# Performance work log

Hardware: AMD Instinct MI355X
Metric: run time of the kernel (lower is better)

The kernel has to match this reference:

```python
import jax, jax.numpy as jnp
import numpy as np

SUPPORT = 1
NEIGHBOR = 20
STRIDE = 2
BS, V = 4, 2048


def _gather(feat, idx):
    # feat: (b, v, c), idx: (b, v, n) -> (b, v, n, c)
    b = feat.shape[0]
    return feat[jnp.arange(b)[:, None, None], idx]


def get_neighbor_index(vertices, k):
    # pairwise squared distances, take k nearest excluding self
    inner = jnp.einsum('bid,bjd->bij', vertices, vertices)
    sq = jnp.sum(vertices * vertices, axis=-1)
    dist = sq[:, :, None] - 2.0 * inner + sq[:, None, :]
    _, idx = jax.lax.top_k(-dist, k + 1)
    return idx[:, :, 1:]


def conv_layer(w, b, d, nbr, vertices, fmap, out_c):
    bs, v, n = nbr.shape
    diff = _gather(vertices, nbr) - vertices[:, :, None, :]  # (b,v,n,3)
    diff = diff / jnp.maximum(jnp.linalg.norm(diff, axis=-1, keepdims=True), 1e-12)
    dirn = d / jnp.maximum(jnp.linalg.norm(d, axis=0, keepdims=True), 1e-12)
    theta = jnp.einsum('bvnd,de->bvne', diff, dirn)  # (b,v,n,S*out)
    feat = fmap @ w + b  # (b,v,(S+1)*out)
    center = feat[..., :out_c]
    support = _gather(feat[..., out_c:], nbr)  # (b,v,n,S*out)
    act = (theta * support).reshape(bs, v, n, SUPPORT, out_c)
    act = jnp.sum(jnp.max(act, axis=2), axis=2)  # max over neighbors, sum over supports
    return center + act


LAYERS = [('c0', 3, 32), ('c1', 32, 64), ('c12', 64, 64), ('c13', 64, 64), ('c14', 64, 64),
          ('p1', 64, 64), ('c2', 64, 128), ('c3', 128, 256), ('c4', 256, 1024),
          ('c42', 1024, 1024), ('c43', 1024, 1024), ('c44', 1024, 1024)]


def _layer_params(key, in_c, out_c):
    k1, k2, k3 = jax.random.split(key, 3)
    stdv = 1.0 / np.sqrt((SUPPORT + 1) * out_c)
    w = jax.random.uniform(k1, (in_c, (SUPPORT + 1) * out_c), minval=-stdv, maxval=stdv, dtype=jnp.float32)
    b = jax.random.uniform(k2, ((SUPPORT + 1) * out_c,), minval=-stdv, maxval=stdv, dtype=jnp.float32)
    d = jax.random.uniform(k3, (3, SUPPORT * out_c), minval=-stdv, maxval=stdv, dtype=jnp.float32)
    return w, b, d


def setup_inputs() -> dict:
    key = jax.random.key(0)
    keys = jax.random.split(key, 20)
    inp = {'vertices': jax.random.normal(keys[0], (BS, V, 3), dtype=jnp.float32)}
    for i, (name, ic, oc) in enumerate(LAYERS):
        w, b, d = _layer_params(keys[i + 1], ic, oc)
        inp[name + '_w'], inp[name + '_b'], inp[name + '_d'] = w, b, d
    inp['fc1_w'] = jax.random.normal(keys[14], (1024, 256), dtype=jnp.float32) * 0.02
    inp['fc1_b'] = jnp.zeros((256,), jnp.float32)
    inp['bn_g'] = jnp.ones((256,), jnp.float32)
    inp['bn_b'] = jnp.zeros((256,), jnp.float32)
    inp['fc2_w'] = jax.random.normal(keys[15], (256, 40), dtype=jnp.float32) * 0.02
    inp['fc2_b'] = jnp.zeros((40,), jnp.float32)
    return inp


def reference(vertices, c0_w, c0_b, c0_d, c1_w, c1_b, c1_d, c12_w, c12_b, c12_d, c13_w, c13_b, c13_d, c14_w, c14_b, c14_d, p1_w, p1_b, p1_d, c2_w, c2_b, c2_d, c3_w, c3_b, c3_d, c4_w, c4_b, c4_d, c42_w, c42_b, c42_d, c43_w, c43_b, c43_d, c44_w, c44_b, c44_d, fc1_w, fc1_b, bn_g, bn_b, fc2_w, fc2_b):
    nbr = get_neighbor_index(vertices, NEIGHBOR)
    fm = conv_layer(c0_w, c0_b, c0_d, nbr, vertices, vertices, 32)
    fm = conv_layer(c1_w, c1_b, c1_d, nbr, vertices, fm, 64)
    fm = conv_layer(c12_w, c12_b, c12_d, nbr, vertices, fm, 64)
    fm = conv_layer(c13_w, c13_b, c13_d, nbr, vertices, fm, 64)
    fm = conv_layer(c14_w, c14_b, c14_d, nbr, vertices, fm, 64)
    # pool_1: conv, neighbor-max pooling, stride-2 vertex subsampling
    fm = conv_layer(p1_w, p1_b, p1_d, nbr, vertices, fm, 64)
    fm = jnp.max(_gather(fm, nbr), axis=2)
    sub = jnp.arange(0, vertices.shape[1], STRIDE)
    vertices2 = vertices[:, sub]
    fm = fm[:, sub]
    nbr2 = get_neighbor_index(vertices2, NEIGHBOR)
    fm = conv_layer(c2_w, c2_b, c2_d, nbr2, vertices2, fm, 128)
    fm = conv_layer(c3_w, c3_b, c3_d, nbr2, vertices2, fm, 256)
    fm = conv_layer(c4_w, c4_b, c4_d, nbr2, vertices2, fm, 1024)
    fm = conv_layer(c42_w, c42_b, c42_d, nbr2, vertices2, fm, 1024)
    fm = conv_layer(c43_w, c43_b, c43_d, nbr2, vertices2, fm, 1024)
    fm = conv_layer(c44_w, c44_b, c44_d, nbr2, vertices2, fm, 1024)
    g = jnp.max(fm, axis=1)  # (b, 1024) global max pool
    h = g @ fc1_w + fc1_b  # dropout = identity in eval
    h = h * jax.lax.rsqrt(jnp.float32(1.0 + 1e-5)) * bn_g + bn_b  # BN eval, running mean 0 / var 1
    h = jax.nn.relu(h)
    return h @ fc2_w + fc2_b
```

## Files before the change

### kernel.cpp

```cpp
#include <hip/hip_runtime.h>
#include <float.h>
#include <math.h>

#define BS 4
#define V1 2048
#define V2 1024
#define NB 20
#define KSEL 21

typedef __attribute__((ext_vector_type(8))) short short8v;
typedef __attribute__((ext_vector_type(4))) float f32x4;

__device__ __forceinline__ unsigned short f2bf(float x) {
    union { float f; unsigned u; } v; v.f = x;
    unsigned r = (v.u + 0x7fffu + ((v.u >> 16) & 1u)) >> 16;
    return (unsigned short)r;
}
__device__ __forceinline__ float bf2f(unsigned short h) {
    return __uint_as_float((unsigned)h << 16);
}
__device__ __forceinline__ unsigned umin32(unsigned a, unsigned b) { return a < b ? a : b; }

__device__ __forceinline__ void gload16(const void* g, void* l) {
    __builtin_amdgcn_global_load_lds((const __attribute__((address_space(1))) void*)g,
                                     (__attribute__((address_space(3))) void*)l, 16, 0, 0);
}

template<int SLOTS>
__global__ __launch_bounds__(256)
void knn_wave_kernel(const float* __restrict__ verts, int stride, int* __restrict__ nbr)
{
    constexpr int Vv = SLOTS * 64;
    __shared__ float xs[Vv], ys[Vv], zs[Vv];
    int tid = threadIdx.x;
    int lane = tid & 63;
    int wv = tid >> 6;
    int b = blockIdx.x / (Vv / 4);
    int q0 = (blockIdx.x % (Vv / 4)) * 4;
    const float* vb = verts + (size_t)b * V1 * 3;
    for (int p = tid; p < Vv; p += 256) {
        xs[p] = vb[(size_t)p * stride * 3 + 0];
        ys[p] = vb[(size_t)p * stride * 3 + 1];
        zs[p] = vb[(size_t)p * stride * 3 + 2];
    }
    __syncthreads();
    int i = q0 + wv;
    float xi = xs[i], yi = ys[i], zi = zs[i];
    float sqi = xi * xi + yi * yi + zi * zi;
    unsigned keys[SLOTS];
    #pragma unroll
    for (int s = 0; s < SLOTS; ++s) {
        int j = s * 64 + lane;
        float xj = xs[j], yj = ys[j], zj = zs[j];
        float sqj = xj * xj + yj * yj + zj * zj;
        float d = sqi - 2.0f * (xi * xj + yi * yj + zi * zj) + sqj;
        unsigned u = __float_as_uint(d);
        u = (u & 0x80000000u) ? ~u : (u | 0x80000000u);
        keys[s] = (u & ~31u) | (unsigned)s;
    }
    const unsigned UMAX = 0xFFFFFFFFu;
    unsigned c0 = UMAX, c1 = UMAX, c2 = UMAX, c3 = UMAX;
    #pragma unroll
    for (int s = 0; s < SLOTS; ++s) c0 = umin32(c0, keys[s]);
    #pragma unroll
    for (int s = 0; s < SLOTS; ++s) { unsigned k = keys[s]; if (k > c0) c1 = umin32(c1, k); }
    #pragma unroll
    for (int s = 0; s < SLOTS; ++s) { unsigned k = keys[s]; if (k > c1) c2 = umin32(c2, k); }
    #pragma unroll
    for (int s = 0; s < SLOTS; ++s) { unsigned k = keys[s]; if (k > c2) c3 = umin32(c3, k); }

    unsigned lm = c0;
    int* out = nbr + ((size_t)b * Vv + i) * NB;
    for (int it = 0; it < KSEL; ++it) {
        unsigned m = lm;
        #pragma unroll
        for (int off = 1; off < 64; off <<= 1)
            m = umin32(m, (unsigned)__shfl_xor((int)m, off));
        unsigned long long bal = __ballot(lm == m);
        int wl = __ffsll(bal) - 1;
        int slot = (int)(m & 31u);
        int j = slot * 64 + wl;
        if (it > 0 && lane == 0) out[it - 1] = j;
        if (lane == wl) {
            c0 = c1; c1 = c2; c2 = c3; c3 = UMAX;
            if (c0 == UMAX) {
                #pragma unroll
                for (int s = 0; s < SLOTS; ++s) {
                    unsigned k = keys[s];
                    if (k > m) c0 = umin32(c0, k);
                }
            }
            lm = c0;
        }
    }
}

__global__ __launch_bounds__(256)
void diffn_kernel(const float* __restrict__ verts, const int* __restrict__ nbr,
                  int Vv, int stride, float* __restrict__ diffn)
{
    int t = blockIdx.x * 256 + threadIdx.x;
    int total = BS * Vv * NB;
    if (t >= total) return;
    int v = (t / NB) % Vv;
    int b = t / (NB * Vv);
    const float* vb = verts + (size_t)b * V1 * 3;
    int j = nbr[t];
    float xi = vb[(size_t)v * stride * 3 + 0];
    float yi = vb[(size_t)v * stride * 3 + 1];
    float zi = vb[(size_t)v * stride * 3 + 2];
    float dx = vb[(size_t)j * stride * 3 + 0] - xi;
    float dy = vb[(size_t)j * stride * 3 + 1] - yi;
    float dz = vb[(size_t)j * stride * 3 + 2] - zi;
    float nrm = sqrtf(dx * dx + dy * dy + dz * dz);
    float inv = 1.0f / fmaxf(nrm, 1e-12f);
    diffn[(size_t)t * 3 + 0] = dx * inv;
    diffn[(size_t)t * 3 + 1] = dy * inv;
    diffn[(size_t)t * 3 + 2] = dz * inv;
}

__global__ __launch_bounds__(256)
void convT_kernel(const float* __restrict__ W, unsigned short* __restrict__ Wt, int K, int N)
{
    __shared__ float t[32][33];
    int k0 = blockIdx.y * 32, n0 = blockIdx.x * 32;
    int tx = threadIdx.x % 32, ty = threadIdx.x / 32;
    #pragma unroll
    for (int r = ty; r < 32; r += 8) t[r][tx] = W[(size_t)(k0 + r) * N + n0 + tx];
    __syncthreads();
    #pragma unroll
    for (int r = ty; r < 32; r += 8) Wt[(size_t)(n0 + r) * K + k0 + tx] = f2bf(t[tx][r]);
}

__global__ __launch_bounds__(256)
void c0_kernel(const float* __restrict__ verts, const float* __restrict__ W,
               const float* __restrict__ Bv, unsigned short* __restrict__ feat)
{
    int t = blockIdx.x * 256 + threadIdx.x;
    if (t >= BS * V1 * 64) return;
    int n = t & 63, m = t >> 6;
    float x = verts[(size_t)m * 3 + 0];
    float y = verts[(size_t)m * 3 + 1];
    float z = verts[(size_t)m * 3 + 2];
    feat[t] = f2bf(x * W[n] + y * W[64 + n] + z * W[128 + n] + Bv[n]);
}

template<int BK>
__global__ __launch_bounds__(256)
void gemm_mfma(const unsigned short* __restrict__ A, const unsigned short* __restrict__ Wt,
               const float* __restrict__ bias, unsigned short* __restrict__ C,
               int M, int N, int K)
{
    constexpr int RB = BK * 2;
    constexpr int TILE_B = 128 * RB;
    constexpr int SWM = (BK == 64) ? 7 : 3;
    __shared__ __align__(16) char smem[2 * TILE_B];
    int tid = threadIdx.x;
    int lane = tid & 63, wid = tid >> 6;
    int wr = wid >> 1, wc = wid & 1;
    int m0 = blockIdx.y * 128, n0 = blockIdx.x * 128;

    f32x4 acc[4][4] = {};

    constexpr int rounds = TILE_B / 4096;
    int srow[rounds], soffe[rounds];
    #pragma unroll
    for (int r = 0; r < rounds; ++r) {
        int L = r * 4096 + tid * 16;
        int row = L / RB;
        int off = (L % RB) ^ ((row & SWM) << 4);
        srow[r] = row; soffe[r] = off >> 1;
    }

    for (int kt = 0; kt < K; kt += BK) {
        #pragma unroll
        for (int r = 0; r < rounds; ++r)
            gload16(A + (size_t)(m0 + srow[r]) * K + kt + soffe[r],
                    smem + r * 4096 + wid * 1024);
        #pragma unroll
        for (int r = 0; r < rounds; ++r)
            gload16(Wt + (size_t)(n0 + srow[r]) * K + kt + soffe[r],
                    smem + TILE_B + r * 4096 + wid * 1024);
        asm volatile("s_waitcnt vmcnt(0)" ::: "memory");
        __syncthreads();
        #pragma unroll
        for (int ks = 0; ks < BK / 32; ++ks) {
            short8v av[4], bv[4];
            #pragma unroll
            for (int i = 0; i < 4; ++i) {
                int row = wr * 64 + i * 16 + (lane & 15);
                int off = (ks * 64 + ((lane >> 4) * 16)) ^ ((row & SWM) << 4);
                av[i] = *(const short8v*)(smem + row * RB + off);
            }
            #pragma unroll
            for (int j = 0; j < 4; ++j) {
                int row = wc * 64 + j * 16 + (lane & 15);
                int off = (ks * 64 + ((lane >> 4) * 16)) ^ ((row & SWM) << 4);
                bv[j] = *(const short8v*)(smem + TILE_B + row * RB + off);
            }
            #pragma unroll
            for (int i = 0; i < 4; ++i)
                #pragma unroll
                for (int j = 0; j < 4; ++j)
                    acc[i][j] = __builtin_amdgcn_mfma_f32_16x16x32_bf16(av[i], bv[j], acc[i][j], 0, 0, 0);
        }
        __syncthreads();
    }
    #pragma unroll
    for (int i = 0; i < 4; ++i) {
        #pragma unroll
        for (int j = 0; j < 4; ++j) {
            int col = n0 + wc * 64 + j * 16 + (lane & 15);
            int rowb = m0 + wr * 64 + i * 16 + ((lane >> 4) * 4);
            float bv2 = bias[col];
            #pragma unroll
            for (int v = 0; v < 4; ++v)
                C[(size_t)(rowb + v) * N + col] = f2bf(acc[i][j][v] + bv2);
        }
    }
}

__global__ __launch_bounds__(256)
void act_kernel(const unsigned short* __restrict__ feat, const int* __restrict__ nbr,
                const float* __restrict__ diffn, const float* __restrict__ dmat,
                float* __restrict__ outp, unsigned short* __restrict__ outh,
                int Vv, int OC)
{
    int OC4 = OC >> 2;
    int t = blockIdx.x * 256 + threadIdx.x;
    int total = BS * Vv * OC4;
    if (t >= total) return;
    int c4 = t % OC4;
    int v = (t / OC4) % Vv;
    int b = t / (OC4 * Vv);
    const float4* d4 = (const float4*)dmat;
    float4 D0 = d4[c4], D1 = d4[OC4 + c4], D2 = d4[2 * OC4 + c4];
    float n0 = sqrtf(D0.x * D0.x + D1.x * D1.x + D2.x * D2.x);
    float n1 = sqrtf(D0.y * D0.y + D1.y * D1.y + D2.y * D2.y);
    float n2 = sqrtf(D0.z * D0.z + D1.z * D1.z + D2.z * D2.z);
    float n3 = sqrtf(D0.w * D0.w + D1.w * D1.w + D2.w * D2.w);
    float i0 = 1.0f / fmaxf(n0, 1e-12f);
    float i1 = 1.0f / fmaxf(n1, 1e-12f);
    float i2 = 1.0f / fmaxf(n2, 1e-12f);
    float i3 = 1.0f / fmaxf(n3, 1e-12f);
    D0.x *= i0; D0.y *= i1; D0.z *= i2; D0.w *= i3;
    D1.x *= i0; D1.y *= i1; D1.z *= i2; D1.w *= i3;
    D2.x *= i0; D2.y *= i1; D2.z *= i2; D2.w *= i3;

    const int* nb = nbr + ((size_t)b * Vv + v) * NB;
    const float* dfn = diffn + ((size_t)b * Vv + v) * NB * 3;
    const ushort4* frow = (const ushort4*)feat;
    size_t rowstride = (size_t)(2 * OC4);
    const ushort4* fsup = frow + (size_t)b * Vv * rowstride + OC4 + c4;
    float4 m = make_float4(-FLT_MAX, -FLT_MAX, -FLT_MAX, -FLT_MAX);
    for (int n = 0; n < NB; ++n) {
        int idx = nb[n];
        float e0 = dfn[3 * n + 0], e1 = dfn[3 * n + 1], e2 = dfn[3 * n + 2];
        ushort4 s = fsup[(size_t)idx * rowstride];
        float th;
        th = e0 * D0.x + e1 * D1.x + e2 * D2.x; m.x = fmaxf(m.x, th * bf2f(s.x));
        th = e0 * D0.y + e1 * D1.y + e2 * D2.y; m.y = fmaxf(m.y, th * bf2f(s.y));
        th = e0 * D0.z + e1 * D1.z + e2 * D2.z; m.z = fmaxf(m.z, th * bf2f(s.z));
        th = e0 * D0.w + e1 * D1.w + e2 * D2.w; m.w = fmaxf(m.w, th * bf2f(s.w));
    }
    ushort4 cen = frow[(size_t)b * Vv * rowstride + (size_t)v * rowstride + c4];
    float4 r = make_float4(bf2f(cen.x) + m.x, bf2f(cen.y) + m.y,
                           bf2f(cen.z) + m.z, bf2f(cen.w) + m.w);
    size_t oidx = ((size_t)b * Vv + v) * OC4 + c4;
    ushort4 h;
    h.x = f2bf(r.x); h.y = f2bf(r.y); h.z = f2bf(r.z); h.w = f2bf(r.w);
    ((ushort4*)outh)[oidx] = h;
    if (outp) ((float4*)outp)[oidx] = r;
}

__global__ __launch_bounds__(256)
void pool_kernel(const ushort4* __restrict__ fmh, const int* __restrict__ nbr,
                 ushort4* __restrict__ outp)
{
    const int C4 = 16;
    int t = blockIdx.x * 256 + threadIdx.x;
    int total = BS * V2 * C4;
    if (t >= total) return;
    int c = t % C4;
    int v2 = (t / C4) % V2;
    int b = t / (C4 * V2);
    const int* nb = nbr + ((size_t)b * V1 + 2 * v2) * NB;
    float4 m = make_float4(-FLT_MAX, -FLT_MAX, -FLT_MAX, -FLT_MAX);
    for (int n = 0; n < NB; ++n) {
        int idx = nb[n];
        ushort4 s = fmh[((size_t)b * V1 + idx) * C4 + c];
        m.x = fmaxf(m.x, bf2f(s.x)); m.y = fmaxf(m.y, bf2f(s.y));
        m.z = fmaxf(m.z, bf2f(s.z)); m.w = fmaxf(m.w, bf2f(s.w));
    }
    ushort4 h;
    h.x = f2bf(m.x); h.y = f2bf(m.y); h.z = f2bf(m.z); h.w = f2bf(m.w);
    outp[((size_t)b * V2 + v2) * C4 + c] = h;
}

__global__ __launch_bounds__(256)
void gmax_part(const float* __restrict__ fm, float* __restrict__ part)
{
    int c = blockIdx.x * 256 + threadIdx.x;
    int ch = blockIdx.y;
    int b = blockIdx.z;
    float m = -FLT_MAX;
    for (int v = ch * 128; v < (ch + 1) * 128; ++v)
        m = fmaxf(m, fm[((size_t)b * V2 + v) * 1024 + c]);
    part[((size_t)b * 8 + ch) * 1024 + c] = m;
}

__global__ __launch_bounds__(256)
void gmax_final(const float* __restrict__ part, float* __restrict__ g)
{
    int t = blockIdx.x * 256 + threadIdx.x;
    if (t >= BS * 1024) return;
    int c = t % 1024, b = t / 1024;
    float m = -FLT_MAX;
    for (int ch = 0; ch < 8; ++ch)
        m = fmaxf(m, part[((size_t)b * 8 + ch) * 1024 + c]);
    g[t] = m;
}

__global__ __launch_bounds__(256)
void fc1_part(const float* __restrict__ g, const float* __restrict__ fc1w,
              float* __restrict__ hpart)
{
    int b = blockIdx.x, kg = blockIdx.y;
    int j = threadIdx.x;
    __shared__ float gs[128];
    if (j < 128) gs[j] = g[(size_t)b * 1024 + kg * 128 + j];
    __syncthreads();
    float h = 0.0f;
    #pragma unroll 4
    for (int k = 0; k < 128; ++k)
        h = fmaf(gs[k], fc1w[(size_t)(kg * 128 + k) * 256 + j], h);
    hpart[((size_t)b * 8 + kg) * 256 + j] = h;
}

__global__ __launch_bounds__(256)
void head2_kernel(const float* __restrict__ hpart, const float* __restrict__ fc1b,
                  const float* __restrict__ bng, const float* __restrict__ bnb,
                  const float* __restrict__ fc2w, const float* __restrict__ fc2b,
                  float* __restrict__ outp)
{
    __shared__ float hs[256];
    __shared__ float part[4][40];
    int b = blockIdx.x;
    int j = threadIdx.x;
    float s = fc1b[j];
    #pragma unroll
    for (int kg = 0; kg < 8; ++kg) s += hpart[((size_t)b * 8 + kg) * 256 + j];
    const float rc = 0.99999500003749937f;
    s = s * rc * bng[j] + bnb[j];
    hs[j] = fmaxf(s, 0.0f);
    __syncthreads();
    int ks = j >> 6, jo = j & 63;
    if (jo < 40) {
        float o = 0.0f;
        for (int k = ks * 64; k < ks * 64 + 64; ++k)
            o = fmaf(hs[k], fc2w[(size_t)k * 40 + jo], o);
        part[ks][jo] = o;
    }
    __syncthreads();
    if (j < 40)
        outp[(size_t)b * 40 + j] = fc2b[j] + part[0][j] + part[1][j] + part[2][j] + part[3][j];
}

extern "C" void kernel_launch(void* const* d_in, const int* in_sizes, int n_in,
                              void* d_out, int out_size, void* d_ws, size_t ws_size,
                              hipStream_t stream)
{
    (void)in_sizes; (void)n_in; (void)out_size; (void)ws_size;
    const float* verts = (const float*)d_in[0];
    auto Wp = [&](int i) { return (const float*)d_in[1 + 3 * i]; };
    auto Bp = [&](int i) { return (const float*)d_in[2 + 3 * i]; };
    auto Dp = [&](int i) { return (const float*)d_in[3 + 3 * i]; };
    const float* fc1w = (const float*)d_in[37];
    const float* fc1b = (const float*)d_in[38];
    const float* bng  = (const float*)d_in[39];
    const float* bnb  = (const float*)d_in[40];
    const float* fc2w = (const float*)d_in[41];
    const float* fc2b = (const float*)d_in[42];

    static const int IC[12] = {3, 32, 64, 64, 64, 64, 64, 128, 256, 1024, 1024, 1024};
    static const int OC[12] = {32, 64, 64, 64, 64, 64, 128, 256, 1024, 1024, 1024, 1024};

    char* ws = (char*)d_ws;
    size_t off = 0;
    auto alloc = [&](size_t bytes) {
        void* p = ws + off;
        off += (bytes + 255) & ~(size_t)255;
        return p;
    };
    int*   nbr1   = (int*)alloc((size_t)BS * V1 * NB * 4);
    int*   nbr2   = (int*)alloc((size_t)BS * V2 * NB * 4);
    float* diffn1 = (float*)alloc((size_t)BS * V1 * NB * 3 * 4);
    float* diffn2 = (float*)alloc((size_t)BS * V2 * NB * 3 * 4);
    unsigned short* feat = (unsigned short*)alloc((size_t)BS * V2 * 2048 * 2);
    unsigned short* fmh0 = (unsigned short*)alloc((size_t)BS * V2 * 1024 * 2);
    unsigned short* fmh1 = (unsigned short*)alloc((size_t)BS * V2 * 1024 * 2);
    float* fm32   = (float*)alloc((size_t)BS * V2 * 1024 * 4);
    float* gpart  = (float*)alloc((size_t)BS * 8 * 1024 * 4);
    float* g      = (float*)alloc((size_t)BS * 1024 * 4);
    float* hpart  = (float*)alloc((size_t)BS * 8 * 256 * 4);

    unsigned short* WtBuf[12];
    {
        size_t total = 0;
        for (int i = 1; i < 12; ++i) total += (size_t)(2 * OC[i]) * IC[i];
        unsigned short* base = (unsigned short*)alloc(total * 2);
        size_t o2 = 0;
        for (int i = 1; i < 12; ++i) { WtBuf[i] = base + o2; o2 += (size_t)(2 * OC[i]) * IC[i]; }
    }
    for (int i = 1; i < 12; ++i) {
        int K = IC[i], N = 2 * OC[i];
        dim3 gdim(N / 32, K / 32);
        convT_kernel<<<gdim, 256, 0, stream>>>(Wp(i), WtBuf[i], K, N);
    }

    auto gemm = [&](const unsigned short* A, int li, unsigned short* Cc, int M) {
        int K = IC[li], N = 2 * OC[li];
        dim3 gdim(N / 128, M / 128);
        if (K % 64 == 0)
            gemm_mfma<64><<<gdim, 256, 0, stream>>>(A, WtBuf[li], Bp(li), Cc, M, N, K);
        else
            gemm_mfma<32><<<gdim, 256, 0, stream>>>(A, WtBuf[li], Bp(li), Cc, M, N, K);
    };
    auto act = [&](const unsigned short* f, const int* nbr, const float* dfn, const float* d,
                   float* outp, unsigned short* outh, int Vv, int oc) {
        int total = BS * Vv * (oc / 4);
        act_kernel<<<(total + 255) / 256, 256, 0, stream>>>(f, nbr, dfn, d, outp, outh, Vv, oc);
    };

    knn_wave_kernel<32><<<BS * V1 / 4, 256, 0, stream>>>(verts, 1, nbr1);
    diffn_kernel<<<(BS * V1 * NB + 255) / 256, 256, 0, stream>>>(verts, nbr1, V1, 1, diffn1);

    c0_kernel<<<(BS * V1 * 64 + 255) / 256, 256, 0, stream>>>(verts, Wp(0), Bp(0), feat);
    unsigned short* hb[2] = {fmh0, fmh1};
    int pb = 0;
    act(feat, nbr1, diffn1, Dp(0), nullptr, hb[pb], V1, OC[0]);
    const unsigned short* cur = hb[pb]; pb ^= 1;

    for (int i = 1; i < 6; ++i) {
        gemm(cur, i, feat, BS * V1);
        act(feat, nbr1, diffn1, Dp(i), nullptr, hb[pb], V1, OC[i]);
        cur = hb[pb]; pb ^= 1;
    }

    {
        int total = BS * V2 * 16;
        pool_kernel<<<(total + 255) / 256, 256, 0, stream>>>(
            (const ushort4*)cur, nbr1, (ushort4*)hb[pb]);
        cur = hb[pb]; pb ^= 1;
    }

    knn_wave_kernel<16><<<BS * V2 / 4, 256, 0, stream>>>(verts, 2, nbr2);
    diffn_kernel<<<(BS * V2 * NB + 255) / 256, 256, 0, stream>>>(verts, nbr2, V2, 2, diffn2);

    for (int i = 6; i < 12; ++i) {
        gemm(cur, i, feat, BS * V2);
        float* f32out = (i == 11) ? fm32 : nullptr;
        act(feat, nbr2, diffn2, Dp(i), f32out, hb[pb], V2, OC[i]);
        cur = hb[pb]; pb ^= 1;
    }

    gmax_part<<<dim3(4, 8, BS), 256, 0, stream>>>(fm32, gpart);
    gmax_final<<<(BS * 1024 + 255) / 256, 256, 0, stream>>>(gpart, g);
    fc1_part<<<dim3(BS, 8), 256, 0, stream>>>(g, fc1w, hpart);
    head2_kernel<<<BS, 256, 0, stream>>>(hpart, fc1b, bng, bnb, fc2w, fc2b, (float*)d_out);
}
```

Baseline: 603.8 us.

## Batch weight transposes, add small GEMM tiles, swizzle blocks, specialize 1024-channel act

Merges the eleven per-layer weight-transpose launches into one kernel that finds its layer from a tile-offset table. The GEMM is templated on tile size, so layers with fewer than 1024 output columns use 64x64 tiles and launch more workgroups. The GEMM also remaps workgroup IDs when the grid size is a multiple of 8. A dedicated 1024-channel activation kernel assigns one vertex per block and interleaves batch and vertex across consecutive blocks. These changes aim to cut launch overhead and raise occupancy on the small layers, at the cost of more template variants and lower per-tile reuse on small GEMMs.

```diff
diff --git a/kernel.cpp b/kernel.cpp
--- a/kernel.cpp
+++ b/kernel.cpp
@@ -119,12 +119,29 @@
     diffn[(size_t)t * 3 + 2] = dz * inv;
 }
 
-__global__ __launch_bounds__(256)
-void convT_kernel(const float* __restrict__ W, unsigned short* __restrict__ Wt, int K, int N)
+struct ConvTArgs {
+    const float* W[11];
+    unsigned short* Wt[11];
+    int K[11];
+    int N[11];
+    int tileoff[12];
+};
+
+__global__ __launch_bounds__(256)
+void convT_all(ConvTArgs a)
 {
     __shared__ float t[32][33];
-    int k0 = blockIdx.y * 32, n0 = blockIdx.x * 32;
-    int tx = threadIdx.x % 32, ty = threadIdx.x / 32;
+    int g = blockIdx.x;
+    int L = 0;
+    #pragma unroll
+    for (int q = 0; q < 10; ++q) if (g >= a.tileoff[q + 1]) L = q + 1;
+    int rel = g - a.tileoff[L];
+    int K = a.K[L], N = a.N[L];
+    int tilesN = N >> 5;
+    int k0 = (rel / tilesN) << 5, n0 = (rel % tilesN) << 5;
+    const float* W = a.W[L];
+    unsigned short* Wt = a.Wt[L];
+    int tx = threadIdx.x & 31, ty = threadIdx.x >> 5;
     #pragma unroll
     for (int r = ty; r < 32; r += 8) t[r][tx] = W[(size_t)(k0 + r) * N + n0 + tx];
     __syncthreads();
@@ -145,27 +162,36 @@
     feat[t] = f2bf(x * W[n] + y * W[64 + n] + z * W[128 + n] + Bv[n]);
 }
 
-template<int BK>
+template<int BK, int BM, int BN>
 __global__ __launch_bounds__(256)
 void gemm_mfma(const unsigned short* __restrict__ A, const unsigned short* __restrict__ Wt,
                const float* __restrict__ bias, unsigned short* __restrict__ C,
                int M, int N, int K)
 {
     constexpr int RB = BK * 2;
-    constexpr int TILE_B = 128 * RB;
+    constexpr int TA = BM * RB;
+    constexpr int TB = BN * RB;
     constexpr int SWM = (BK == 64) ? 7 : 3;
-    __shared__ __align__(16) char smem[2 * TILE_B];
+    constexpr int FI = BM / 32, FJ = BN / 32;
+    constexpr int RA = TA / 4096, RBN = TB / 4096;
+    constexpr int RMAX = (RA > RBN) ? RA : RBN;
+    __shared__ __align__(16) char smem[TA + TB];
     int tid = threadIdx.x;
     int lane = tid & 63, wid = tid >> 6;
     int wr = wid >> 1, wc = wid & 1;
-    int m0 = blockIdx.y * 128, n0 = blockIdx.x * 128;
-
-    f32x4 acc[4][4] = {};
-
-    constexpr int rounds = TILE_B / 4096;
-    int srow[rounds], soffe[rounds];
-    #pragma unroll
-    for (int r = 0; r < rounds; ++r) {
+
+    int nwg = gridDim.x * gridDim.y;
+    int orig = blockIdx.y * gridDim.x + blockIdx.x;
+    int wg = orig;
+    if ((nwg & 7) == 0) wg = (orig & 7) * (nwg >> 3) + (orig >> 3);
+    int m0 = (wg / gridDim.x) * BM;
+    int n0 = (wg % gridDim.x) * BN;
+
+    f32x4 acc[FI][FJ] = {};
+
+    int srow[RMAX], soffe[RMAX];
+    #pragma unroll
+    for (int r = 0; r < RMAX; ++r) {
         int L = r * 4096 + tid * 16;
         int row = L / RB;
         int off = (L % RB) ^ ((row & SWM) << 4);
@@ -174,44 +200,44 @@
 
     for (int kt = 0; kt < K; kt += BK) {
         #pragma unroll
-        for (int r = 0; r < rounds; ++r)
+        for (int r = 0; r < RA; ++r)
             gload16(A + (size_t)(m0 + srow[r]) * K + kt + soffe[r],
                     smem + r * 4096 + wid * 1024);
         #pragma unroll
-        for (int r = 0; r < rounds; ++r)
+        for (int r = 0; r < RBN; ++r)
             gload16(Wt + (size_t)(n0 + srow[r]) * K + kt + soffe[r],
-                    smem + TILE_B + r * 4096 + wid * 1024);
+                    smem + TA + r * 4096 + wid * 1024);
         asm volatile("s_waitcnt vmcnt(0)" ::: "memory");
         __syncthreads();
         #pragma unroll
         for (int ks = 0; ks < BK / 32; ++ks) {
-            short8v av[4], bv[4];
+            short8v av[FI], bv[FJ];
             #pragma unroll
-            for (int i = 0; i < 4; ++i) {
-                int row = wr * 64 + i * 16 + (lane & 15);
+            for (int i = 0; i < FI; ++i) {
+                int row = wr * (BM / 2) + i * 16 + (lane & 15);
                 int off = (ks * 64 + ((lane >> 4) * 16)) ^ ((row & SWM) << 4);
                 av[i] = *(const short8v*)(smem + row * RB + off);
             }
             #pragma unroll
-            for (int j = 0; j < 4; ++j) {
-                int row = wc * 64 + j * 16 + (lane & 15);
+            for (int j = 0; j < FJ; ++j) {
+                int row = wc * (BN / 2) + j * 16 + (lane & 15);
                 int off = (ks * 64 + ((lane >> 4) * 16)) ^ ((row & SWM) << 4);
-                bv[j] = *(const short8v*)(smem + TILE_B + row * RB + off);
+                bv[j] = *(const short8v*)(smem + TA + row * RB + off);
             }
             #pragma unroll
-            for (int i = 0; i < 4; ++i)
+            for (int i = 0; i < FI; ++i)
                 #pragma unroll
-                for (int j = 0; j < 4; ++j)
+                for (int j = 0; j < FJ; ++j)
                     acc[i][j] = __builtin_amdgcn_mfma_f32_16x16x32_bf16(av[i], bv[j], acc[i][j], 0, 0, 0);
         }
         __syncthreads();
     }
     #pragma unroll
-    for (int i = 0; i < 4; ++i) {
+    for (int i = 0; i < FI; ++i) {
         #pragma unroll
-        for (int j = 0; j < 4; ++j) {
-            int col = n0 + wc * 64 + j * 16 + (lane & 15);
-            int rowb = m0 + wr * 64 + i * 16 + ((lane >> 4) * 4);
+        for (int j = 0; j < FJ; ++j) {
+            int col = n0 + wc * (BN / 2) + j * 16 + (lane & 15);
+            int rowb = m0 + wr * (BM / 2) + i * 16 + ((lane >> 4) * 4);
             float bv2 = bias[col];
             #pragma unroll
             for (int v = 0; v < 4; ++v)
@@ -274,6 +300,56 @@
 }
 
 __global__ __launch_bounds__(256)
+void act1024_kernel(const unsigned short* __restrict__ feat, const int* __restrict__ nbr,
+                    const float* __restrict__ diffn, const float* __restrict__ dmat,
+                    float* __restrict__ outp, unsigned short* __restrict__ outh)
+{
+    const int OC4 = 256;
+    int g = blockIdx.x;
+    int b = (g & 7) >> 1;
+    int v = ((g >> 3) << 1) | (g & 1);
+    int c4 = threadIdx.x;
+    const float4* d4 = (const float4*)dmat;
+    float4 D0 = d4[c4], D1 = d4[OC4 + c4], D2 = d4[2 * OC4 + c4];
+    float n0 = sqrtf(D0.x * D0.x + D1.x * D1.x + D2.x * D2.x);
+    float n1 = sqrtf(D0.y * D0.y + D1.y * D1.y + D2.y * D2.y);
+    float n2 = sqrtf(D0.z * D0.z + D1.z * D1.z + D2.z * D2.z);
+    float n3 = sqrtf(D0.w * D0.w + D1.w * D1.w + D2.w * D2.w);
+    float i0 = 1.0f / fmaxf(n0, 1e-12f);
+    float i1 = 1.0f / fmaxf(n1, 1e-12f);
+    float i2 = 1.0f / fmaxf(n2, 1e-12f);
+    float i3 = 1.0f / fmaxf(n3, 1e-12f);
+    D0.x *= i0; D0.y *= i1; D0.z *= i2; D0.w *= i3;
+    D1.x *= i0; D1.y *= i1; D1.z *= i2; D1.w *= i3;
+    D2.x *= i0; D2.y *= i1; D2.z *= i2; D2.w *= i3;
+
+    const int* nb = nbr + ((size_t)b * V2 + v) * NB;
+    const float* dfn = diffn + ((size_t)b * V2 + v) * NB * 3;
+    const ushort4* frow = (const ushort4*)feat;
+    const size_t rowstride = 2 * OC4;
+    const ushort4* fsup = frow + (size_t)b * V2 * rowstride + OC4 + c4;
+    float4 m = make_float4(-FLT_MAX, -FLT_MAX, -FLT_MAX, -FLT_MAX);
+    for (int n = 0; n < NB; ++n) {
+        int idx = nb[n];
+        float e0 = dfn[3 * n + 0], e1 = dfn[3 * n + 1], e2 = dfn[3 * n + 2];
+        ushort4 s = fsup[(size_t)idx * rowstride];
+        float th;
+        th = e0 * D0.x + e1 * D1.x + e2 * D2.x; m.x = fmaxf(m.x, th * bf2f(s.x));
+        th = e0 * D0.y + e1 * D1.y + e2 * D2.y; m.y = fmaxf(m.y, th * bf2f(s.y));
+        th = e0 * D0.z + e1 * D1.z + e2 * D2.z; m.z = fmaxf(m.z, th * bf2f(s.z));
+        th = e0 * D0.w + e1 * D1.w + e2 * D2.w; m.w = fmaxf(m.w, th * bf2f(s.w));
+    }
+    ushort4 cen = frow[((size_t)b * V2 + v) * rowstride + c4];
+    float4 r = make_float4(bf2f(cen.x) + m.x, bf2f(cen.y) + m.y,
+                           bf2f(cen.z) + m.z, bf2f(cen.w) + m.w);
+    size_t oidx = ((size_t)b * V2 + v) * OC4 + c4;
+    ushort4 h;
+    h.x = f2bf(r.x); h.y = f2bf(r.y); h.z = f2bf(r.z); h.w = f2bf(r.w);
+    ((ushort4*)outh)[oidx] = h;
+    if (outp) ((float4*)outp)[oidx] = r;
+}
+
+__global__ __launch_bounds__(256)
 void pool_kernel(const ushort4* __restrict__ fmh, const int* __restrict__ nbr,
                  ushort4* __restrict__ outp)
 {
@@ -412,24 +488,43 @@
         size_t o2 = 0;
         for (int i = 1; i < 12; ++i) { WtBuf[i] = base + o2; o2 += (size_t)(2 * OC[i]) * IC[i]; }
     }
-    for (int i = 1; i < 12; ++i) {
-        int K = IC[i], N = 2 * OC[i];
-        dim3 gdim(N / 32, K / 32);
-        convT_kernel<<<gdim, 256, 0, stream>>>(Wp(i), WtBuf[i], K, N);
+    {
+        ConvTArgs a;
+        int toff = 0;
+        for (int i = 1; i < 12; ++i) {
+            int K = IC[i], N = 2 * OC[i];
+            a.W[i - 1] = Wp(i);
+            a.Wt[i - 1] = WtBuf[i];
+            a.K[i - 1] = K;
+            a.N[i - 1] = N;
+            a.tileoff[i - 1] = toff;
+            toff += (K / 32) * (N / 32);
+        }
+        a.tileoff[11] = toff;
+        convT_all<<<toff, 256, 0, stream>>>(a);
     }
 
     auto gemm = [&](const unsigned short* A, int li, unsigned short* Cc, int M) {
         int K = IC[li], N = 2 * OC[li];
-        dim3 gdim(N / 128, M / 128);
-        if (K % 64 == 0)
-            gemm_mfma<64><<<gdim, 256, 0, stream>>>(A, WtBuf[li], Bp(li), Cc, M, N, K);
-        else
-            gemm_mfma<32><<<gdim, 256, 0, stream>>>(A, WtBuf[li], Bp(li), Cc, M, N, K);
+        if (N >= 1024) {
+            dim3 gdim(N / 128, M / 128);
+            gemm_mfma<64, 128, 128><<<gdim, 256, 0, stream>>>(A, WtBuf[li], Bp(li), Cc, M, N, K);
+        } else if (K % 64 == 0) {
+            dim3 gdim(N / 64, M / 64);
+            gemm_mfma<64, 64, 64><<<gdim, 256, 0, stream>>>(A, WtBuf[li], Bp(li), Cc, M, N, K);
+        } else {
+            dim3 gdim(N / 64, M / 64);
+            gemm_mfma<32, 64, 64><<<gdim, 256, 0, stream>>>(A, WtBuf[li], Bp(li), Cc, M, N, K);
+        }
     };
     auto act = [&](const unsigned short* f, const int* nbr, const float* dfn, const float* d,
                    float* outp, unsigned short* outh, int Vv, int oc) {
-        int total = BS * Vv * (oc / 4);
-        act_kernel<<<(total + 255) / 256, 256, 0, stream>>>(f, nbr, dfn, d, outp, outh, Vv, oc);
+        if (oc == 1024) {
+            act1024_kernel<<<BS * V2, 256, 0, stream>>>(f, nbr, dfn, d, outp, outh);
+        } else {
+            int total = BS * Vv * (oc / 4);
+            act_kernel<<<(total + 255) / 256, 256, 0, stream>>>(f, nbr, dfn, d, outp, outh, Vv, oc);
+        }
     };
 
     knn_wave_kernel<32><<<BS * V1 / 4, 256, 0, stream>>>(verts, 1, nbr1);
```

After: 521.0 us. 1.16x faster.
